# Performance work log

Measured on AMD Instinct MI355X. Metric: run time of the kernel, lower is better.

Reference implementation:

```python
import jax, jax.numpy as jnp
import numpy as np

B, C_IN, C_OUT, H, W_SP = 64, 256, 256, 32, 32
G = H * W_SP  # groups == H*W per module assert


def setup_inputs() -> dict:
    key = jax.random.key(0)
    k1, k2, k3 = jax.random.split(key, 3)
    x = jax.random.normal(k1, (B, C_IN, H, W_SP), dtype=jnp.float32)
    # grouped 1x1 conv == per-group linear: weight [G, C_out, C_in], bias [G, C_out]
    W = jax.random.normal(k2, (G, C_OUT, C_IN), dtype=jnp.float32) * (1.0 / np.sqrt(C_IN))
    b = jax.random.normal(k3, (G, C_OUT), dtype=jnp.float32) * 0.01
    return {"x": x, "W": W, "b": b}


def reference(x, W, b):
    Bn, Cin, Hn, Wn = x.shape
    Gn = Hn * Wn
    # permute(0,2,3,1).reshape(B,-1,1,1): channels-last flatten -> [B, G, C_in]
    xg = jnp.transpose(x, (0, 2, 3, 1)).reshape(Bn, Gn, Cin)
    # block-diagonal batched matmul per spatial position (group)
    out = jnp.einsum("bgi,goi->bgo", xg, W) + b  # [B, G, C_out]
    # view(B,H,W,C_out).permute(0,3,1,2)
    return jnp.transpose(out.reshape(Bn, Hn, Wn, -1), (0, 3, 1, 2))
```

## Files before the change

### kernel.cpp

```cpp
#include <hip/hip_runtime.h>
#include <hip/hip_bf16.h>

typedef __bf16 bf16x8 __attribute__((ext_vector_type(8)));
typedef float f32x4 __attribute__((ext_vector_type(4)));

#define GN   1024
#define BATCH 64
#define CIN  256
#define COUT 256

static __device__ __forceinline__ ushort f2bf(float f) {
  __hip_bfloat16 h = __float2bfloat16(f);
  return *reinterpret_cast<ushort*>(&h);
}
static __device__ __forceinline__ float bf2f(ushort u) {
  uint v = (uint)u << 16;
  return *reinterpret_cast<float*>(&v);
}

__global__ __launch_bounds__(256) void k_transpose_convert(
    const float* __restrict__ x, ushort* __restrict__ xT)
{
  __shared__ float tile[64][65];
  const int g0 = blockIdx.x * 64;
  const int i0 = blockIdx.y * 64;
  const int b  = blockIdx.z;
  const int t  = threadIdx.x;
  const int a  = t & 15;
  const int r  = t >> 4;

  const float* xb = x + (size_t)b * CIN * GN;
#pragma unroll
  for (int p = 0; p < 4; ++p) {
    int ii = p * 16 + r;
    float4 v = *reinterpret_cast<const float4*>(
        &xb[(size_t)(i0 + ii) * GN + g0 + a * 4]);
    tile[ii][a * 4 + 0] = v.x;
    tile[ii][a * 4 + 1] = v.y;
    tile[ii][a * 4 + 2] = v.z;
    tile[ii][a * 4 + 3] = v.w;
  }
  __syncthreads();

  ushort* xTb = xT + (size_t)b * GN * CIN;
#pragma unroll
  for (int p = 0; p < 4; ++p) {
    int gg = p * 16 + r;
    ushort4 u;
    u.x = f2bf(tile[a * 4 + 0][gg]);
    u.y = f2bf(tile[a * 4 + 1][gg]);
    u.z = f2bf(tile[a * 4 + 2][gg]);
    u.w = f2bf(tile[a * 4 + 3][gg]);
    *reinterpret_cast<ushort4*>(&xTb[(size_t)(g0 + gg) * CIN + i0 + a * 4]) = u;
  }
}

__global__ __launch_bounds__(256) void k_group_gemm(
    const ushort* __restrict__ xT, const float* __restrict__ W,
    const float* __restrict__ bias, float* __restrict__ out,
    ushort* __restrict__ outT, int use_ws)
{
  const int g    = blockIdx.x;
  const int tid  = threadIdx.x;
  const int wave = tid >> 6;
  const int lane = tid & 63;

  __shared__ __align__(16) ushort lA[BATCH * CIN];

#pragma unroll
  for (int r = 0; r < 8; ++r) {
    int b = r * 8 + (tid >> 5);
    int i = (tid & 31) * 8;
    int4 v = *reinterpret_cast<const int4*>(xT + ((size_t)b * GN + g) * CIN + i);
    *reinterpret_cast<int4*>(&lA[b * CIN + (i ^ ((b & 7) << 3))]) = v;
  }
  __syncthreads();

  const int oc = (wave << 6) + (lane & 15);
  const int kq = (lane >> 4) << 3;

  const float* wptr[4];
#pragma unroll
  for (int n = 0; n < 4; ++n)
    wptr[n] = W + ((size_t)g * COUT + oc + n * 16) * CIN + kq;

  f32x4 acc[4][4];
#pragma unroll
  for (int m = 0; m < 4; ++m)
#pragma unroll
    for (int n = 0; n < 4; ++n)
      acc[m][n] = {0.f, 0.f, 0.f, 0.f};

  float4 bnext[4][2];
#pragma unroll
  for (int n = 0; n < 4; ++n) {
    bnext[n][0] = *reinterpret_cast<const float4*>(wptr[n]);
    bnext[n][1] = *reinterpret_cast<const float4*>(wptr[n] + 4);
  }

#pragma unroll
  for (int ks = 0; ks < 8; ++ks) {
    float4 bcur[4][2];
#pragma unroll
    for (int n = 0; n < 4; ++n) {
      bcur[n][0] = bnext[n][0];
      bcur[n][1] = bnext[n][1];
    }
    if (ks < 7) {
#pragma unroll
      for (int n = 0; n < 4; ++n) {
        bnext[n][0] = *reinterpret_cast<const float4*>(wptr[n] + (ks + 1) * 32);
        bnext[n][1] = *reinterpret_cast<const float4*>(wptr[n] + (ks + 1) * 32 + 4);
      }
    }

    bf16x8 bfr[4];
#pragma unroll
    for (int n = 0; n < 4; ++n) {
      bfr[n][0] = (__bf16)bcur[n][0].x;
      bfr[n][1] = (__bf16)bcur[n][0].y;
      bfr[n][2] = (__bf16)bcur[n][0].z;
      bfr[n][3] = (__bf16)bcur[n][0].w;
      bfr[n][4] = (__bf16)bcur[n][1].x;
      bfr[n][5] = (__bf16)bcur[n][1].y;
      bfr[n][6] = (__bf16)bcur[n][1].z;
      bfr[n][7] = (__bf16)bcur[n][1].w;
    }

    bf16x8 afr[4];
    const int i0 = ks * 32 + kq;
#pragma unroll
    for (int m = 0; m < 4; ++m) {
      int row = m * 16 + (lane & 15);
      afr[m] = *reinterpret_cast<const bf16x8*>(
          &lA[row * CIN + (i0 ^ ((row & 7) << 3))]);
    }

    __builtin_amdgcn_s_setprio(1);
#pragma unroll
    for (int m = 0; m < 4; ++m)
#pragma unroll
      for (int n = 0; n < 4; ++n)
        acc[m][n] = __builtin_amdgcn_mfma_f32_16x16x32_bf16(
            afr[m], bfr[n], acc[m][n], 0, 0, 0);
    __builtin_amdgcn_s_setprio(0);
  }

  float bv[4];
#pragma unroll
  for (int n = 0; n < 4; ++n) bv[n] = bias[g * COUT + oc + n * 16];

  if (use_ws) {
#pragma unroll
    for (int m = 0; m < 4; ++m) {
#pragma unroll
      for (int n = 0; n < 4; ++n) {
        int o = oc + n * 16;
#pragma unroll
        for (int j = 0; j < 4; ++j) {
          int b = m * 16 + ((lane >> 4) << 2) + j;
          __hip_bfloat16 h = __float2bfloat16(acc[m][n][j] + bv[n]);
          outT[((size_t)b * GN + g) * COUT + o] = *reinterpret_cast<ushort*>(&h);
        }
      }
    }
  } else {
#pragma unroll
    for (int m = 0; m < 4; ++m) {
#pragma unroll
      for (int n = 0; n < 4; ++n) {
        int o = oc + n * 16;
#pragma unroll
        for (int j = 0; j < 4; ++j) {
          int b = m * 16 + ((lane >> 4) << 2) + j;
          out[((size_t)b * COUT + o) * GN + g] = acc[m][n][j] + bv[n];
        }
      }
    }
  }
}

__global__ __launch_bounds__(256) void k_transpose_out(
    const ushort* __restrict__ outT, float* __restrict__ out)
{
  __shared__ float tile[64][65];
  const int g0 = blockIdx.x * 64;
  const int o0 = blockIdx.y * 64;
  const int b  = blockIdx.z;
  const int t  = threadIdx.x;
  const int a  = t & 15;
  const int r  = t >> 4;

  const ushort* src = outT + (size_t)b * GN * COUT;
#pragma unroll
  for (int p = 0; p < 4; ++p) {
    int gl = p * 16 + r;
    ushort4 u = *reinterpret_cast<const ushort4*>(
        &src[(size_t)(g0 + gl) * COUT + o0 + a * 4]);
    tile[gl][a * 4 + 0] = bf2f(u.x);
    tile[gl][a * 4 + 1] = bf2f(u.y);
    tile[gl][a * 4 + 2] = bf2f(u.z);
    tile[gl][a * 4 + 3] = bf2f(u.w);
  }
  __syncthreads();

  float* dst = out + (size_t)b * COUT * GN;
#pragma unroll
  for (int p = 0; p < 4; ++p) {
    int ol = p * 16 + r;
    float4 v;
    v.x = tile[a * 4 + 0][ol];
    v.y = tile[a * 4 + 1][ol];
    v.z = tile[a * 4 + 2][ol];
    v.w = tile[a * 4 + 3][ol];
    *reinterpret_cast<float4*>(&dst[(size_t)(o0 + ol) * GN + g0 + a * 4]) = v;
  }
}

extern "C" void kernel_launch(void* const* d_in, const int* in_sizes, int n_in,
                              void* d_out, int out_size, void* d_ws, size_t ws_size,
                              hipStream_t stream) {
  const float* x  = (const float*)d_in[0];
  const float* W  = (const float*)d_in[1];
  const float* bs = (const float*)d_in[2];
  float* out      = (float*)d_out;

  const size_t xT_elems = (size_t)BATCH * GN * CIN;
  const size_t oT_elems = (size_t)BATCH * GN * COUT;
  const bool use_ws = ws_size >= (xT_elems + oT_elems) * sizeof(ushort);

  ushort* xT   = (ushort*)d_ws;
  ushort* outT = xT + xT_elems;

  dim3 grid1(GN / 64, CIN / 64, BATCH);
  k_transpose_convert<<<grid1, 256, 0, stream>>>(x, xT);
  k_group_gemm<<<GN, 256, 0, stream>>>(xT, W, bs, out,
                                       use_ws ? outT : nullptr,
                                       use_ws ? 1 : 0);
  if (use_ws) {
    dim3 grid3(GN / 64, COUT / 64, BATCH);
    k_transpose_out<<<grid3, 256, 0, stream>>>(outT, out);
  }
}
```

Measured before the change: 122.6 us.

## Stage weights and activations into LDS via async global_load_lds double buffering

The grouped GEMM kernel now loads the activation tile and per-wave weight slices straight into LDS with global_load_lds, using a swizzled layout and double-buffered weight stages gated by explicit vmcnt waits. To match the direct copy, the transpose kernel now writes xT already XOR-swizzled. The aim is to overlap weight streaming with MFMA work and cut VGPR pressure from register prefetch. In exchange, LDS use per block rises to about 96KB, which may reduce occupancy, and correctness depends on hand-counted waitcnt values and swizzle consistency.

```diff
diff --git a/kernel.cpp b/kernel.cpp
--- a/kernel.cpp
+++ b/kernel.cpp
@@ -4,10 +4,18 @@
 typedef __bf16 bf16x8 __attribute__((ext_vector_type(8)));
 typedef float f32x4 __attribute__((ext_vector_type(4)));
 
-#define GN   1024
+#define GN    1024
 #define BATCH 64
-#define CIN  256
-#define COUT 256
+#define CIN   256
+#define COUT  256
+#define WSLICE 8192
+
+#define G_AS __attribute__((address_space(1)))
+#define L_AS __attribute__((address_space(3)))
+
+static __device__ __forceinline__ void gload16(const void* g, void* l) {
+  __builtin_amdgcn_global_load_lds((const G_AS void*)g, (L_AS void*)l, 16, 0, 0);
+}
 
 static __device__ __forceinline__ ushort f2bf(float f) {
   __hip_bfloat16 h = __float2bfloat16(f);
@@ -28,6 +36,7 @@
   const int t  = threadIdx.x;
   const int a  = t & 15;
   const int r  = t >> 4;
+  const int key = (b & 7) << 3;
 
   const float* xb = x + (size_t)b * CIN * GN;
 #pragma unroll
@@ -51,7 +60,8 @@
     u.y = f2bf(tile[a * 4 + 1][gg]);
     u.z = f2bf(tile[a * 4 + 2][gg]);
     u.w = f2bf(tile[a * 4 + 3][gg]);
-    *reinterpret_cast<ushort4*>(&xTb[(size_t)(g0 + gg) * CIN + i0 + a * 4]) = u;
+    int isw = (i0 + a * 4) ^ key;
+    *reinterpret_cast<ushort4*>(&xTb[(size_t)(g0 + gg) * CIN + isw]) = u;
   }
 }
 
@@ -60,29 +70,45 @@
     const float* __restrict__ bias, float* __restrict__ out,
     ushort* __restrict__ outT, int use_ws)
 {
+  __shared__ __align__(16) unsigned char lds[BATCH * CIN * 2 + 4 * 2 * WSLICE];
+  ushort* lA        = (ushort*)lds;
+  unsigned char* lW = lds + BATCH * CIN * 2;
+
   const int g    = blockIdx.x;
   const int tid  = threadIdx.x;
   const int wave = tid >> 6;
   const int lane = tid & 63;
 
-  __shared__ __align__(16) ushort lA[BATCH * CIN];
-
-#pragma unroll
-  for (int r = 0; r < 8; ++r) {
-    int b = r * 8 + (tid >> 5);
-    int i = (tid & 31) * 8;
-    int4 v = *reinterpret_cast<const int4*>(xT + ((size_t)b * GN + g) * CIN + i);
-    *reinterpret_cast<int4*>(&lA[b * CIN + (i ^ ((b & 7) << 3))]) = v;
-  }
-  __syncthreads();
-
-  const int oc = (wave << 6) + (lane & 15);
-  const int kq = (lane >> 4) << 3;
-
-  const float* wptr[4];
-#pragma unroll
-  for (int n = 0; n < 4; ++n)
-    wptr[n] = W + ((size_t)g * COUT + oc + n * 16) * CIN + kq;
+#pragma unroll
+  for (int j = 0; j < 8; ++j) {
+    int b = 16 * wave + 2 * j + (lane >> 5);
+    const ushort* gsrc = xT + ((size_t)b * GN + g) * CIN + (lane & 31) * 8;
+    ushort* ldst = lA + (16 * wave + 2 * j) * CIN;
+    gload16(gsrc, ldst);
+  }
+
+  const float* wg = W + ((size_t)g * COUT + 64 * wave) * CIN;
+  const int swz_src = ((lane & 7) ^ (lane >> 3)) << 4;
+  const int wrow    = lane >> 3;
+
+  auto stage_w = [&](int ks, int buf) {
+    unsigned char* ldb = lW + wave * (2 * WSLICE) + buf * WSLICE;
+    const unsigned char* gb = (const unsigned char*)wg + (size_t)ks * 128 + swz_src;
+#pragma unroll
+    for (int j = 0; j < 8; ++j) {
+      gload16(gb + (size_t)(8 * j + wrow) * (CIN * 4), ldb + j * 1024);
+    }
+  };
+
+  stage_w(0, 0);
+  stage_w(1, 1);
+  asm volatile("s_waitcnt vmcnt(16)" ::: "memory");
+  __builtin_amdgcn_sched_barrier(0);
+  __builtin_amdgcn_s_barrier();
+
+  const int arow = lane & 15;
+  const int colk = (lane >> 4) * 32;
+  const int kq   = (lane >> 4) << 3;
 
   f32x4 acc[4][4];
 #pragma unroll
@@ -91,47 +117,32 @@
     for (int n = 0; n < 4; ++n)
       acc[m][n] = {0.f, 0.f, 0.f, 0.f};
 
-  float4 bnext[4][2];
-#pragma unroll
-  for (int n = 0; n < 4; ++n) {
-    bnext[n][0] = *reinterpret_cast<const float4*>(wptr[n]);
-    bnext[n][1] = *reinterpret_cast<const float4*>(wptr[n] + 4);
-  }
-
 #pragma unroll
   for (int ks = 0; ks < 8; ++ks) {
-    float4 bcur[4][2];
+    if (ks < 7) { asm volatile("s_waitcnt vmcnt(8)" ::: "memory"); }
+    else        { asm volatile("s_waitcnt vmcnt(0)" ::: "memory"); }
+    __builtin_amdgcn_sched_barrier(0);
+
+    unsigned char* wb = lW + wave * (2 * WSLICE) + (ks & 1) * WSLICE;
+
+    bf16x8 bfr[4];
 #pragma unroll
     for (int n = 0; n < 4; ++n) {
-      bcur[n][0] = bnext[n][0];
-      bcur[n][1] = bnext[n][1];
-    }
-    if (ks < 7) {
-#pragma unroll
-      for (int n = 0; n < 4; ++n) {
-        bnext[n][0] = *reinterpret_cast<const float4*>(wptr[n] + (ks + 1) * 32);
-        bnext[n][1] = *reinterpret_cast<const float4*>(wptr[n] + (ks + 1) * 32 + 4);
-      }
-    }
-
-    bf16x8 bfr[4];
-#pragma unroll
-    for (int n = 0; n < 4; ++n) {
-      bfr[n][0] = (__bf16)bcur[n][0].x;
-      bfr[n][1] = (__bf16)bcur[n][0].y;
-      bfr[n][2] = (__bf16)bcur[n][0].z;
-      bfr[n][3] = (__bf16)bcur[n][0].w;
-      bfr[n][4] = (__bf16)bcur[n][1].x;
-      bfr[n][5] = (__bf16)bcur[n][1].y;
-      bfr[n][6] = (__bf16)bcur[n][1].z;
-      bfr[n][7] = (__bf16)bcur[n][1].w;
+      int row = n * 16 + arow;
+      int key = (row & 7) << 4;
+      float4 f0 = *reinterpret_cast<const float4*>(wb + row * 128 + (colk ^ key));
+      float4 f1 = *reinterpret_cast<const float4*>(wb + row * 128 + ((colk + 16) ^ key));
+      bfr[n][0] = (__bf16)f0.x; bfr[n][1] = (__bf16)f0.y;
+      bfr[n][2] = (__bf16)f0.z; bfr[n][3] = (__bf16)f0.w;
+      bfr[n][4] = (__bf16)f1.x; bfr[n][5] = (__bf16)f1.y;
+      bfr[n][6] = (__bf16)f1.z; bfr[n][7] = (__bf16)f1.w;
     }
 
     bf16x8 afr[4];
     const int i0 = ks * 32 + kq;
 #pragma unroll
     for (int m = 0; m < 4; ++m) {
-      int row = m * 16 + (lane & 15);
+      int row = m * 16 + arow;
       afr[m] = *reinterpret_cast<const bf16x8*>(
           &lA[row * CIN + (i0 ^ ((row & 7) << 3))]);
     }
@@ -144,8 +155,15 @@
         acc[m][n] = __builtin_amdgcn_mfma_f32_16x16x32_bf16(
             afr[m], bfr[n], acc[m][n], 0, 0, 0);
     __builtin_amdgcn_s_setprio(0);
-  }
-
+
+    if (ks < 6) {
+      asm volatile("s_waitcnt lgkmcnt(0)" ::: "memory");
+      __builtin_amdgcn_sched_barrier(0);
+      stage_w(ks + 2, ks & 1);
+    }
+  }
+
+  const int oc = 64 * wave + arow;
   float bv[4];
 #pragma unroll
   for (int n = 0; n < 4; ++n) bv[n] = bias[g * COUT + oc + n * 16];
```

After: 116.4 us. 1.05x faster.
